# Optimization experiments

Measured on AMD Instinct MI355X. Metric: run time of the kernel, lower is better.

## Reference

```python
import jax, jax.numpy as jnp
import numpy as np

HIDDEN = 1024
INTER = 4096
N_EXPERTS = 8


def geglu(x, w1, w2, w3):
    # x: [N, C], w1/w2: [C, I], w3: [I, C]
    return (jax.nn.gelu(x @ w1, approximate=False) * (x @ w2)) @ w3


def setup_inputs() -> dict:
    key = jax.random.key(0)
    ks = jax.random.split(key, 8)
    s = 0.02
    x = jax.random.normal(ks[0], (2, 2048, HIDDEN), dtype=jnp.float32)
    w1s = jax.random.normal(ks[1], (HIDDEN, INTER), dtype=jnp.float32) * s
    w2s = jax.random.normal(ks[2], (HIDDEN, INTER), dtype=jnp.float32) * s
    w3s = jax.random.normal(ks[3], (INTER, HIDDEN), dtype=jnp.float32) * s
    W1 = jax.random.normal(ks[4], (N_EXPERTS, HIDDEN, INTER), dtype=jnp.float32) * s
    W2 = jax.random.normal(ks[5], (N_EXPERTS, HIDDEN, INTER), dtype=jnp.float32) * s
    W3 = jax.random.normal(ks[6], (N_EXPERTS, INTER, HIDDEN), dtype=jnp.float32) * s
    Wg = jax.random.normal(ks[7], (HIDDEN, N_EXPERTS), dtype=jnp.float32) * s
    return {"x": x, "w1s": w1s, "w2s": w2s, "w3s": w3s,
            "W1": W1, "W2": W2, "W3": W3, "Wg": Wg}


def reference(x, w1s, w2s, w3s, W1, W2, W3, Wg):
    B, T, C = x.shape
    xf = x.reshape(-1, C)  # [N, C]
    shared = geglu(xf, w1s, w2s, w3s)  # [N, C]
    logits = xf @ Wg  # [N, E]
    # top-1 of softmax == argmax of logits (softmax is monotone);
    # NOTE: original torch code does NOT multiply by the routing prob.
    idx = jnp.argmax(logits, axis=-1)  # [N]
    final = jnp.zeros_like(xf)
    for e in range(N_EXPERTS):  # small fixed expert count
        y = geglu(xf, W1[e], W2[e], W3[e])  # [N, C]
        final = final + jnp.where((idx == e)[:, None], y, 0.0)
    return (shared + final).reshape(B, T, C)
```

## Files before the change

### kernel.cpp

```cpp
#include <hip/hip_runtime.h>
#include <stdint.h>

#define HIDDEN 1024
#define INTER  4096
#define NTOK   4096
#define HROWS  (2*NTOK)
#define MAXB1  40
#define MAXB2  72
#define NMAT   27

typedef unsigned short u16;
typedef unsigned int   u32;
typedef __bf16  bf16x8 __attribute__((ext_vector_type(8)));
typedef float   f32x4  __attribute__((ext_vector_type(4)));
typedef u32     u32x4  __attribute__((ext_vector_type(4)));

#define WAITVM(N) asm volatile("s_waitcnt vmcnt(" #N ")" ::: "memory")

__device__ __forceinline__ void hard_barrier() {
  asm volatile("" ::: "memory");
  __builtin_amdgcn_s_barrier();
  asm volatile("" ::: "memory");
}

__device__ __forceinline__ u16 f2bf(float f) {
  u32 u = __float_as_uint(f);
  u32 r = u + 0x7FFFu + ((u >> 16) & 1u);
  return (u16)(r >> 16);
}

__device__ __forceinline__ u32 cvt_pk_bf16(float lo, float hi) {
  u32 r;
  asm("v_cvt_pk_bf16_f32 %0, %1, %2" : "=v"(r) : "v"(lo), "v"(hi));
  return r;
}

__device__ __forceinline__ void glds16(const void* g, void* l) {
  __builtin_amdgcn_global_load_lds(
      (const __attribute__((address_space(1))) void*)g,
      (__attribute__((address_space(3))) void*)l, 16, 0, 0);
}


__global__ void k_init(int* cnt, int* fill) {
  if (threadIdx.x < 8) { cnt[threadIdx.x] = 0; fill[threadIdx.x] = 0; }
}

__global__ __launch_bounds__(256) void k_gate(const float* __restrict__ x,
                                              const float* __restrict__ wg,
                                              int* __restrict__ idx,
                                              int* __restrict__ cnt) {
  int wave = threadIdx.x >> 6, lane = threadIdx.x & 63;
  int t = blockIdx.x * 4 + wave;
  if (t >= NTOK) return;
  float acc[8];
  #pragma unroll
  for (int e = 0; e < 8; ++e) acc[e] = 0.f;
  const float* xr = x + (size_t)t * HIDDEN;
  for (int c = lane; c < HIDDEN; c += 64) {
    float xv = xr[c];
    const float* wrow = wg + (size_t)c * 8;
    #pragma unroll
    for (int e = 0; e < 8; ++e) acc[e] += xv * wrow[e];
  }
  #pragma unroll
  for (int e = 0; e < 8; ++e)
    for (int s = 32; s; s >>= 1) acc[e] += __shfl_xor(acc[e], s);
  if (lane == 0) {
    int best = 0; float bv = acc[0];
    #pragma unroll
    for (int e = 1; e < 8; ++e) if (acc[e] > bv) { bv = acc[e]; best = e; }
    idx[t] = best;
    atomicAdd(&cnt[best], 1);
  }
}

__global__ void k_cvt(const float* __restrict__ x, u16* __restrict__ xb, int n4) {
  int i = blockIdx.x * blockDim.x + threadIdx.x;
  if (i >= n4) return;
  float4 v = ((const float4*)x)[i];
  ushort4 o;
  o.x = f2bf(v.x); o.y = f2bf(v.y); o.z = f2bf(v.z); o.w = f2bf(v.w);
  ((ushort4*)xb)[i] = o;
}

__global__ void k_table(const int* __restrict__ cnt, int* __restrict__ off,
                        int4* __restrict__ tab1, int* __restrict__ nblk1,
                        int4* __restrict__ tab2, int* __restrict__ nblk2) {
  if (threadIdx.x != 0 || blockIdx.x != 0) return;
  int o = 0;
  int offs[8];
  for (int e = 0; e < 8; ++e) { offs[e] = o; off[e] = o; o += cnt[e]; }
  int nb = 0;
  for (int m = 0; m < NTOK / 256; ++m)
    tab1[nb++] = make_int4(8, m * 256, 256, 0);
  for (int e = 0; e < 8; ++e)
    for (int j = 0; j * 256 < cnt[e]; ++j) {
      int rows = cnt[e] - j * 256; if (rows > 256) rows = 256;
      tab1[nb++] = make_int4(e, NTOK + offs[e] + j * 256, rows, offs[e] + j * 256);
    }
  *nblk1 = nb;
  nb = 0;
  for (int m = 0; m < NTOK / 128; ++m)
    tab2[nb++] = make_int4(8, m * 128, 128, 0);
  for (int e = 0; e < 8; ++e)
    for (int j = 0; j * 128 < cnt[e]; ++j) {
      int rows = cnt[e] - j * 128; if (rows > 128) rows = 128;
      tab2[nb++] = make_int4(e, NTOK + offs[e] + j * 128, rows, offs[e] + j * 128);
    }
  *nblk2 = nb;
}

__global__ void k_scatter(const int* __restrict__ idx, const int* __restrict__ off,
                          int* __restrict__ fill, int* __restrict__ perm) {
  int t = blockIdx.x * blockDim.x + threadIdx.x;
  if (t >= NTOK) return;
  int e = idx[t];
  int p = atomicAdd(&fill[e], 1);
  perm[off[e] + p] = t;
}


__global__ __launch_bounds__(256) void k_wcvt(
    const float* __restrict__ w1s, const float* __restrict__ w2s,
    const float* __restrict__ w3s, const float* __restrict__ W1,
    const float* __restrict__ W2,  const float* __restrict__ W3,
    u16* __restrict__ Wb)
{
  int bid = blockIdx.x;
  int m = bid >> 9, pair = bid & 511;
  const float* src; int N, nkt, kt, pp2;
  if (m < 18) {
    N = INTER; nkt = 32;
    int mm = (m < 9) ? m : m - 9;
    const float* sp = (m < 9) ? w1s : w2s;
    const float* ep = (m < 9) ? W1 : W2;
    src = (mm == 0) ? sp : ep + (size_t)(mm - 1) * HIDDEN * INTER;
    kt = pair >> 4; pp2 = pair & 15;
  } else {
    N = HIDDEN; nkt = 128;
    int mm = m - 18;
    src = (mm == 0) ? w3s : W3 + (size_t)(mm - 1) * INTER * HIDDEN;
    kt = pair >> 2; pp2 = pair & 3;
  }

  __shared__ float tileF[32 * 256];
  int tid = threadIdx.x;
  const float* in0 = src + (size_t)(kt * 32) * N + pp2 * 256;
  #pragma unroll
  for (int i = 0; i < 8; ++i) {
    int f = tid + 256 * i;
    int k = f >> 6, c4 = f & 63;
    *(float4*)&tileF[k * 256 + c4 * 4] = *(const float4*)(in0 + (size_t)k * N + c4 * 4);
  }
  __syncthreads();

  int p2 = tid >> 7, n = tid & 127;
  int pidx = m * 1024 + (pp2 * 2 + p2) * nkt + kt;
  u16* outp = Wb + (size_t)pidx * 4096 + n * 32;
  #pragma unroll
  for (int s = 0; s < 4; ++s) {
    int k8 = s ^ ((n >> 1) & 3);
    const float* col = &tileF[(k8 * 8) * 256 + p2 * 128 + n];
    u32x4 pk;
    pk.x = cvt_pk_bf16(col[0],    col[256]);
    pk.y = cvt_pk_bf16(col[512],  col[768]);
    pk.z = cvt_pk_bf16(col[1024], col[1280]);
    pk.w = cvt_pk_bf16(col[1536], col[1792]);
    *(u32x4*)(outp + s * 8) = pk;
  }
}


#define MLP1_TILE(B, STG, WN)                                                        \
  do {                                                                               \
    const u16* LA = pAr  + (B) * 16384;                                              \
    const u16* L1 = pBr1 + (B) * 16384;                                              \
    const u16* L2 = pBr2 + (B) * 16384;                                              \
    bf16x8 af[8], f1[2], f2[2];                                                      \
    _Pragma("unroll")                                                                \
    for (int mi = 0; mi < 4; ++mi) af[mi] = *(const bf16x8*)(LA + mi * 512);         \
    _Pragma("unroll")                                                                \
    for (int ni = 0; ni < 2; ++ni) {                                                 \
      f1[ni] = *(const bf16x8*)(L1 + ni * 512);                                      \
      f2[ni] = *(const bf16x8*)(L2 + ni * 512);                                      \
    }                                                                                \
    if (STG) {                                                                       \
      char* Ld = smem + (((B) + 3) & 3) * 32768;                                     \
      glds16(srcA0, Ld + w * 2048);                                                  \
      glds16(srcA1, Ld + w * 2048 + 1024);                                           \
      srcA0 += 64; srcA1 += 64;                                                      \
    }                                                                                \
    __builtin_amdgcn_s_setprio(1);                                                   \
    _Pragma("unroll")                                                                \
    for (int mi = 0; mi < 4; ++mi) {                                                 \
      acc1[mi][0] = __builtin_amdgcn_mfma_f32_16x16x32_bf16(af[mi], f1[0], acc1[mi][0], 0, 0, 0); \
      acc1[mi][1] = __builtin_amdgcn_mfma_f32_16x16x32_bf16(af[mi], f1[1], acc1[mi][1], 0, 0, 0); \
      acc2[mi][0] = __builtin_amdgcn_mfma_f32_16x16x32_bf16(af[mi], f2[0], acc2[mi][0], 0, 0, 0); \
      acc2[mi][1] = __builtin_amdgcn_mfma_f32_16x16x32_bf16(af[mi], f2[1], acc2[mi][1], 0, 0, 0); \
    }                                                                                \
    __builtin_amdgcn_s_setprio(0);                                                   \
    hard_barrier();                                                                  \
    _Pragma("unroll")                                                                \
    for (int mi = 4; mi < 8; ++mi) af[mi] = *(const bf16x8*)(LA + mi * 512);         \
    if (STG) {                                                                       \
      char* Ld = smem + (((B) + 3) & 3) * 32768;                                     \
      glds16(srcB1, Ld + 16384 + w * 1024);                                          \
      glds16(srcB2, Ld + 24576 + w * 1024);                                          \
      srcB1 += 8192; srcB2 += 8192;                                                  \
    }                                                                                \
    __builtin_amdgcn_s_setprio(1);                                                   \
    _Pragma("unroll")                                                                \
    for (int mi = 4; mi < 8; ++mi) {                                                 \
      acc1[mi][0] = __builtin_amdgcn_mfma_f32_16x16x32_bf16(af[mi], f1[0], acc1[mi][0], 0, 0, 0); \
      acc1[mi][1] = __builtin_amdgcn_mfma_f32_16x16x32_bf16(af[mi], f1[1], acc1[mi][1], 0, 0, 0); \
      acc2[mi][0] = __builtin_amdgcn_mfma_f32_16x16x32_bf16(af[mi], f2[0], acc2[mi][0], 0, 0, 0); \
      acc2[mi][1] = __builtin_amdgcn_mfma_f32_16x16x32_bf16(af[mi], f2[1], acc2[mi][1], 0, 0, 0); \
    }                                                                                \
    __builtin_amdgcn_s_setprio(0);                                                   \
    WN;                                                                              \
    hard_barrier();                                                                  \
  } while (0)

__global__ __launch_bounds__(512, 2) void k_mlp1(
    const u16* __restrict__ xb, const u16* __restrict__ Wb,
    const int* __restrict__ perm, const int4* __restrict__ tab,
    const int* __restrict__ nblk, u16* __restrict__ Hbuf)
{
  int bx = blockIdx.x;
  if (bx >= *nblk) return;
  int4 te = tab[bx];
  int g = te.x, hrow0 = te.y, rows = te.z, pb = te.w;
  int m1 = (g == 8) ? 0 : 1 + g;
  int pp = blockIdx.y;
  int nbase = pp * 128;

  extern __shared__ __align__(16) char smem[];
  int tid = threadIdx.x;
  int w = tid >> 6, lane = tid & 63;
  int q = lane >> 4, rl = lane & 15;
  int mw = w >> 2, nw = w & 3;

  int tokj[2];
  #pragma unroll
  for (int j = 0; j < 2; ++j) {
    int r = w * 32 + j * 16 + (lane >> 2);
    int rc = (r < rows) ? r : (rows - 1);
    tokj[j] = (g == 8) ? (hrow0 + rc) : perm[pb + rc];
  }
  int gch = ((lane & 3) ^ ((lane >> 3) & 3)) * 16;

  const char* srcA0 = (const char*)xb + (size_t)tokj[0] * 2048 + gch;
  const char* srcA1 = (const char*)xb + (size_t)tokj[1] * 2048 + gch;
  const char* srcB1 = (const char*)Wb + ((size_t)m1 * 1024 + pp * 32) * 8192 + (tid << 4);
  const char* srcB2 = (const char*)Wb + ((size_t)(m1 + 9) * 1024 + pp * 32) * 8192 + (tid << 4);

  int co = (q ^ ((rl >> 1) & 3)) * 8;
  const u16* pAr  = (const u16*)smem + (mw * 128 + rl) * 32 + co;
  const u16* pBr1 = (const u16*)smem + 8192  + (nw * 32 + rl) * 32 + co;
  const u16* pBr2 = (const u16*)smem + 12288 + (nw * 32 + rl) * 32 + co;

  f32x4 acc1[8][2], acc2[8][2];
  f32x4 z = {0.f, 0.f, 0.f, 0.f};
  #pragma unroll
  for (int mi = 0; mi < 8; ++mi)
    #pragma unroll
    for (int ni = 0; ni < 2; ++ni) { acc1[mi][ni] = z; acc2[mi][ni] = z; }

  #pragma unroll
  for (int p = 0; p < 3; ++p) {
    char* Ld = smem + p * 32768;
    glds16(srcA0, Ld + w * 2048);
    glds16(srcA1, Ld + w * 2048 + 1024);
    srcA0 += 64; srcA1 += 64;
    glds16(srcB1, Ld + 16384 + w * 1024);
    glds16(srcB2, Ld + 24576 + w * 1024);
    srcB1 += 8192; srcB2 += 8192;
  }
  WAITVM(8);
  hard_barrier();

  for (int t0 = 0; t0 < 28; t0 += 4) {
    MLP1_TILE(0, 1, WAITVM(8));
    MLP1_TILE(1, 1, WAITVM(8));
    MLP1_TILE(2, 1, WAITVM(8));
    MLP1_TILE(3, 1, WAITVM(8));
  }
  MLP1_TILE(0, 1, WAITVM(8));
  MLP1_TILE(1, 0, WAITVM(4));
  MLP1_TILE(2, 0, WAITVM(0));
  MLP1_TILE(3, 0, (void)0);

  #pragma unroll
  for (int mi = 0; mi < 8; ++mi) {
    #pragma unroll
    for (int j = 0; j < 4; ++j) {
      int r = mw * 128 + mi * 16 + q * 4 + j;
      if (r < rows) {
        size_t hb = (size_t)(hrow0 + r) * INTER + nbase + nw * 32;
        #pragma unroll
        for (int ni = 0; ni < 2; ++ni) {
          float h1 = acc1[mi][ni][j];
          float h2 = acc2[mi][ni][j];
          float ge = 0.5f * h1 * (1.0f + erff(h1 * 0.7071067811865476f));
          Hbuf[hb + ni * 16 + rl] = f2bf(ge * h2);
        }
      }
    }
  }
}


#define MLP2_TILE(B, STG, WN)                                                        \
  do {                                                                               \
    const u16* LA = pAr + (B) * 12288;                                               \
    const u16* LB = pBr + (B) * 12288;                                               \
    bf16x8 af[4], bf[4];                                                             \
    _Pragma("unroll")                                                                \
    for (int mi = 0; mi < 4; ++mi) af[mi] = *(const bf16x8*)(LA + mi * 512);         \
    _Pragma("unroll")                                                                \
    for (int ni = 0; ni < 4; ++ni) bf[ni] = *(const bf16x8*)(LB + ni * 512);         \
    if (STG) {                                                                       \
      char* Ld = smem + (((B) + 3) & 3) * 24576;                                     \
      glds16(srcA0, Ld + w * 1024);              srcA0 += 64;                        \
      glds16(srcB0, Ld + 8192 + w * 1024);       srcB0 += 8192;                      \
      glds16(srcB1, Ld + 16384 + w * 1024);      srcB1 += 8192;                      \
    }                                                                                \
    __builtin_amdgcn_s_setprio(1);                                                   \
    _Pragma("unroll")                                                                \
    for (int mi = 0; mi < 4; ++mi)                                                   \
      _Pragma("unroll")                                                              \
      for (int ni = 0; ni < 4; ++ni)                                                 \
        acc[mi][ni] = __builtin_amdgcn_mfma_f32_16x16x32_bf16(af[mi], bf[ni], acc[mi][ni], 0, 0, 0); \
    __builtin_amdgcn_s_setprio(0);                                                   \
    WN;                                                                              \
    hard_barrier();                                                                  \
  } while (0)

__global__ __launch_bounds__(512, 2) void k_mlp2(
    const u16* __restrict__ Hbuf, const u16* __restrict__ Wb,
    const int* __restrict__ perm, const int4* __restrict__ tab,
    const int* __restrict__ nblk, float* __restrict__ out,
    float* __restrict__ yexp)
{
  int bx = blockIdx.x;
  if (bx >= *nblk) return;
  int4 te = tab[bx];
  int g = te.x, hrow0 = te.y, rows = te.z, pb = te.w;
  int m3 = (g == 8) ? 18 : 19 + g;
  int pp2 = blockIdx.y;

  extern __shared__ __align__(16) char smem[];
  int tid = threadIdx.x;
  int w = tid >> 6, lane = tid & 63;
  int q = lane >> 4, rl = lane & 15;
  int mw = w >> 2, nw = w & 3;

  int rr = w * 16 + (lane >> 2);
  int rc = (rr < rows) ? rr : (rows - 1);
  int hr = hrow0 + rc;
  int gch = ((lane & 3) ^ ((lane >> 3) & 3)) * 16;

  const char* srcA0 = (const char*)Hbuf + (size_t)hr * (INTER * 2) + gch;
  const char* srcB0 = (const char*)Wb + ((size_t)m3 * 1024 + (pp2 * 2) * 128) * 8192 + (tid << 4);
  const char* srcB1 = (const char*)Wb + ((size_t)m3 * 1024 + (pp2 * 2 + 1) * 128) * 8192 + (tid << 4);

  int co = (q ^ ((rl >> 1) & 3)) * 8;
  const u16* pAr = (const u16*)smem + (mw * 64 + rl) * 32 + co;
  const u16* pBr = (const u16*)smem + 4096 + (nw * 64 + rl) * 32 + co;

  f32x4 acc[4][4];
  f32x4 z = {0.f, 0.f, 0.f, 0.f};
  #pragma unroll
  for (int mi = 0; mi < 4; ++mi)
    #pragma unroll
    for (int ni = 0; ni < 4; ++ni) acc[mi][ni] = z;

  #pragma unroll
  for (int p = 0; p < 3; ++p) {
    char* Ld = smem + p * 24576;
    glds16(srcA0, Ld + w * 1024);          srcA0 += 64;
    glds16(srcB0, Ld + 8192 + w * 1024);   srcB0 += 8192;
    glds16(srcB1, Ld + 16384 + w * 1024);  srcB1 += 8192;
  }
  WAITVM(6);
  hard_barrier();

  for (int t0 = 0; t0 < 124; t0 += 4) {
    MLP2_TILE(0, 1, WAITVM(6));
    MLP2_TILE(1, 1, WAITVM(6));
    MLP2_TILE(2, 1, WAITVM(6));
    MLP2_TILE(3, 1, WAITVM(6));
  }
  MLP2_TILE(0, 1, WAITVM(6));
  MLP2_TILE(1, 0, WAITVM(3));
  MLP2_TILE(2, 0, WAITVM(0));
  MLP2_TILE(3, 0, (void)0);

  float* dstb = (g == 8) ? out : yexp;
  #pragma unroll
  for (int mi = 0; mi < 4; ++mi) {
    #pragma unroll
    for (int j = 0; j < 4; ++j) {
      int r = mw * 64 + mi * 16 + q * 4 + j;
      if (r < rows) {
        int tok = (g == 8) ? (hrow0 + r) : perm[pb + r];
        size_t ob = (size_t)tok * HIDDEN + pp2 * 256 + nw * 64;
        #pragma unroll
        for (int ni = 0; ni < 4; ++ni)
          dstb[ob + ni * 16 + rl] = acc[mi][ni][j];
      }
    }
  }
}

__global__ void k_add(float* __restrict__ out, const float* __restrict__ yexp, int n4) {
  int i = blockIdx.x * blockDim.x + threadIdx.x;
  if (i >= n4) return;
  float4 a = ((const float4*)out)[i];
  float4 b = ((const float4*)yexp)[i];
  a.x += b.x; a.y += b.y; a.z += b.z; a.w += b.w;
  ((float4*)out)[i] = a;
}


extern "C" void kernel_launch(void* const* d_in, const int* in_sizes, int n_in,
                              void* d_out, int out_size, void* d_ws, size_t ws_size,
                              hipStream_t stream) {
  const float* x   = (const float*)d_in[0];
  const float* w1s = (const float*)d_in[1];
  const float* w2s = (const float*)d_in[2];
  const float* w3s = (const float*)d_in[3];
  const float* W1  = (const float*)d_in[4];
  const float* W2  = (const float*)d_in[5];
  const float* W3  = (const float*)d_in[6];
  const float* Wg  = (const float*)d_in[7];
  float* out = (float*)d_out;

  char* ws = (char*)d_ws;
  size_t o_xb   = 0;
  size_t o_H    = o_xb   + (size_t)NTOK * HIDDEN * 2;
  size_t o_yexp = o_H    + (size_t)HROWS * INTER * 2;
  size_t o_Wb   = o_yexp + (size_t)NTOK * HIDDEN * 4;
  size_t o_idx  = o_Wb   + (size_t)NMAT * 1024 * 8192;
  size_t o_perm = o_idx  + (size_t)NTOK * 4;
  size_t o_cnt  = o_perm + (size_t)NTOK * 4;
  size_t o_off  = o_cnt  + 32;
  size_t o_fill = o_off  + 32;
  size_t o_nb1  = o_fill + 32;
  size_t o_nb2  = o_nb1  + 32;
  size_t o_tab1 = o_nb2  + 32;
  size_t o_tab2 = o_tab1 + (size_t)MAXB1 * 16;
  size_t need   = o_tab2 + (size_t)MAXB2 * 16;
  if (ws_size < need) return;

  u16*  xb   = (u16*)(ws + o_xb);
  u16*  Hbuf = (u16*)(ws + o_H);
  float* yexp = (float*)(ws + o_yexp);
  u16*  Wb   = (u16*)(ws + o_Wb);
  int*  idx  = (int*)(ws + o_idx);
  int*  perm = (int*)(ws + o_perm);
  int*  cnt  = (int*)(ws + o_cnt);
  int*  off  = (int*)(ws + o_off);
  int*  fill = (int*)(ws + o_fill);
  int*  nblk1 = (int*)(ws + o_nb1);
  int*  nblk2 = (int*)(ws + o_nb2);
  int4* tab1 = (int4*)(ws + o_tab1);
  int4* tab2 = (int4*)(ws + o_tab2);

  k_init<<<1, 64, 0, stream>>>(cnt, fill);
  k_gate<<<NTOK / 4, 256, 0, stream>>>(x, Wg, idx, cnt);
  k_cvt<<<(NTOK * HIDDEN / 4) / 256, 256, 0, stream>>>(x, xb, NTOK * HIDDEN / 4);
  k_wcvt<<<NMAT * 512, 256, 0, stream>>>(w1s, w2s, w3s, W1, W2, W3, Wb);
  k_table<<<1, 1, 0, stream>>>(cnt, off, tab1, nblk1, tab2, nblk2);
  k_scatter<<<NTOK / 256, 256, 0, stream>>>(idx, off, fill, perm);
  k_mlp1<<<dim3(MAXB1, INTER / 128), 512, 131072, stream>>>(xb, Wb, perm, tab1, nblk1, Hbuf);
  k_mlp2<<<dim3(MAXB2, HIDDEN / 256), 512, 98304, stream>>>(Hbuf, Wb, perm, tab2, nblk2, out, yexp);
  k_add<<<(NTOK * HIDDEN / 4) / 256, 256, 0, stream>>>(out, yexp, NTOK * HIDDEN / 4);
}
```

Baseline: 524.0 us.

## Prefetch next-stage LDS fragments into registers and tighten vmcnt waits in MLP kernels

Both GEMM kernels now load the next k-stage's LDS operand fragments into registers during the current stage's MFMAs. k_mlp1 staggers the A/B fragment reads across the barrier halves, and k_mlp2 ping-pongs two register fragment sets. The vmcnt waits are tightened so the next staged buffer is ready before it is read ahead. This aims to hide LDS read latency behind MFMA execution, at the cost of higher register pressure that could hurt occupancy at launch_bounds(512,2).

```diff
diff --git a/kernel.cpp b/kernel.cpp
--- a/kernel.cpp
+++ b/kernel.cpp
@@ -172,19 +172,17 @@
 }
 
 
-#define MLP1_TILE(B, STG, WN)                                                        \
+#define M1_TILE(B, STG, RD, WN)                                                      \
   do {                                                                               \
-    const u16* LA = pAr  + (B) * 16384;                                              \
-    const u16* L1 = pBr1 + (B) * 16384;                                              \
-    const u16* L2 = pBr2 + (B) * 16384;                                              \
-    bf16x8 af[8], f1[2], f2[2];                                                      \
-    _Pragma("unroll")                                                                \
-    for (int mi = 0; mi < 4; ++mi) af[mi] = *(const bf16x8*)(LA + mi * 512);         \
-    _Pragma("unroll")                                                                \
-    for (int ni = 0; ni < 2; ++ni) {                                                 \
-      f1[ni] = *(const bf16x8*)(L1 + ni * 512);                                      \
-      f2[ni] = *(const bf16x8*)(L2 + ni * 512);                                      \
-    }                                                                                \
+    const u16* LA  = pAr  + (B) * 16384;                                             \
+    const u16* LAn = pAr  + (((B) + 1) & 3) * 16384;                                 \
+    const u16* L1n = pBr1 + (((B) + 1) & 3) * 16384;                                 \
+    const u16* L2n = pBr2 + (((B) + 1) & 3) * 16384;                                 \
+                            \
+    af[4] = *(const bf16x8*)(LA + 4 * 512);                                          \
+    af[5] = *(const bf16x8*)(LA + 5 * 512);                                          \
+    af[6] = *(const bf16x8*)(LA + 6 * 512);                                          \
+    af[7] = *(const bf16x8*)(LA + 7 * 512);                                          \
     if (STG) {                                                                       \
       char* Ld = smem + (((B) + 3) & 3) * 32768;                                     \
       glds16(srcA0, Ld + w * 2048);                                                  \
@@ -201,8 +199,13 @@
     }                                                                                \
     __builtin_amdgcn_s_setprio(0);                                                   \
     hard_barrier();                                                                  \
-    _Pragma("unroll")                                                                \
-    for (int mi = 4; mi < 8; ++mi) af[mi] = *(const bf16x8*)(LA + mi * 512);         \
+          \
+    if (RD) {                                                                        \
+      af[0] = *(const bf16x8*)(LAn);                                                 \
+      af[1] = *(const bf16x8*)(LAn + 512);                                           \
+      af[2] = *(const bf16x8*)(LAn + 2 * 512);                                       \
+      af[3] = *(const bf16x8*)(LAn + 3 * 512);                                       \
+    }                                                                                \
     if (STG) {                                                                       \
       char* Ld = smem + (((B) + 3) & 3) * 32768;                                     \
       glds16(srcB1, Ld + 16384 + w * 1024);                                          \
@@ -218,6 +221,13 @@
       acc2[mi][1] = __builtin_amdgcn_mfma_f32_16x16x32_bf16(af[mi], f2[1], acc2[mi][1], 0, 0, 0); \
     }                                                                                \
     __builtin_amdgcn_s_setprio(0);                                                   \
+    \
+    if (RD) {                                                                        \
+      f1[0] = *(const bf16x8*)(L1n);                                                 \
+      f1[1] = *(const bf16x8*)(L1n + 512);                                           \
+      f2[0] = *(const bf16x8*)(L2n);                                                 \
+      f2[1] = *(const bf16x8*)(L2n + 512);                                           \
+    }                                                                                \
     WN;                                                                              \
     hard_barrier();                                                                  \
   } while (0)
@@ -277,19 +287,29 @@
     glds16(srcB2, Ld + 24576 + w * 1024);
     srcB1 += 8192; srcB2 += 8192;
   }
-  WAITVM(8);
+  WAITVM(4);
   hard_barrier();
 
-  for (int t0 = 0; t0 < 28; t0 += 4) {
-    MLP1_TILE(0, 1, WAITVM(8));
-    MLP1_TILE(1, 1, WAITVM(8));
-    MLP1_TILE(2, 1, WAITVM(8));
-    MLP1_TILE(3, 1, WAITVM(8));
-  }
-  MLP1_TILE(0, 1, WAITVM(8));
-  MLP1_TILE(1, 0, WAITVM(4));
-  MLP1_TILE(2, 0, WAITVM(0));
-  MLP1_TILE(3, 0, (void)0);
+  bf16x8 af[8], f1[2], f2[2];
+  af[0] = *(const bf16x8*)(pAr);
+  af[1] = *(const bf16x8*)(pAr + 512);
+  af[2] = *(const bf16x8*)(pAr + 2 * 512);
+  af[3] = *(const bf16x8*)(pAr + 3 * 512);
+  f1[0] = *(const bf16x8*)(pBr1);
+  f1[1] = *(const bf16x8*)(pBr1 + 512);
+  f2[0] = *(const bf16x8*)(pBr2);
+  f2[1] = *(const bf16x8*)(pBr2 + 512);
+
+  for (int t0 = 0; t0 < 7; ++t0) {
+    M1_TILE(0, 1, 1, WAITVM(4));
+    M1_TILE(1, 1, 1, WAITVM(4));
+    M1_TILE(2, 1, 1, WAITVM(4));
+    M1_TILE(3, 1, 1, WAITVM(4));
+  }
+  M1_TILE(0, 1, 1, WAITVM(4));
+  M1_TILE(1, 0, 1, WAITVM(0));
+  M1_TILE(2, 0, 1, (void)0);
+  M1_TILE(3, 0, 0, (void)0);
 
   #pragma unroll
   for (int mi = 0; mi < 8; ++mi) {
@@ -311,15 +331,20 @@
 }
 
 
-#define MLP2_TILE(B, STG, WN)                                                        \
+#define M2_TILE(B, CUR, NXT, STG, RD, WN)                                            \
   do {                                                                               \
-    const u16* LA = pAr + (B) * 12288;                                               \
-    const u16* LB = pBr + (B) * 12288;                                               \
-    bf16x8 af[4], bf[4];                                                             \
-    _Pragma("unroll")                                                                \
-    for (int mi = 0; mi < 4; ++mi) af[mi] = *(const bf16x8*)(LA + mi * 512);         \
-    _Pragma("unroll")                                                                \
-    for (int ni = 0; ni < 4; ++ni) bf[ni] = *(const bf16x8*)(LB + ni * 512);         \
+    const u16* LAn = pAr + (((B) + 1) & 3) * 12288;                                  \
+    const u16* LBn = pBr + (((B) + 1) & 3) * 12288;                                  \
+    if (RD) {                                                                        \
+      af##NXT[0] = *(const bf16x8*)(LAn);                                            \
+      af##NXT[1] = *(const bf16x8*)(LAn + 512);                                      \
+      af##NXT[2] = *(const bf16x8*)(LAn + 2 * 512);                                  \
+      af##NXT[3] = *(const bf16x8*)(LAn + 3 * 512);                                  \
+      bf##NXT[0] = *(const bf16x8*)(LBn);                                            \
+      bf##NXT[1] = *(const bf16x8*)(LBn + 512);                                      \
+      bf##NXT[2] = *(const bf16x8*)(LBn + 2 * 512);                                  \
+      bf##NXT[3] = *(const bf16x8*)(LBn + 3 * 512);                                  \
+    }                                                                                \
     if (STG) {                                                                       \
       char* Ld = smem + (((B) + 3) & 3) * 24576;                                     \
       glds16(srcA0, Ld + w * 1024);              srcA0 += 64;                        \
@@ -331,7 +356,7 @@
     for (int mi = 0; mi < 4; ++mi)                                                   \
       _Pragma("unroll")                                                              \
       for (int ni = 0; ni < 4; ++ni)                                                 \
-        acc[mi][ni] = __builtin_amdgcn_mfma_f32_16x16x32_bf16(af[mi], bf[ni], acc[mi][ni], 0, 0, 0); \
+        acc[mi][ni] = __builtin_amdgcn_mfma_f32_16x16x32_bf16(af##CUR[mi], bf##CUR[ni], acc[mi][ni], 0, 0, 0); \
     __builtin_amdgcn_s_setprio(0);                                                   \
     WN;                                                                              \
     hard_barrier();                                                                  \
@@ -383,19 +408,29 @@
     glds16(srcB0, Ld + 8192 + w * 1024);   srcB0 += 8192;
     glds16(srcB1, Ld + 16384 + w * 1024);  srcB1 += 8192;
   }
-  WAITVM(6);
+  WAITVM(3);
   hard_barrier();
 
-  for (int t0 = 0; t0 < 124; t0 += 4) {
-    MLP2_TILE(0, 1, WAITVM(6));
-    MLP2_TILE(1, 1, WAITVM(6));
-    MLP2_TILE(2, 1, WAITVM(6));
-    MLP2_TILE(3, 1, WAITVM(6));
-  }
-  MLP2_TILE(0, 1, WAITVM(6));
-  MLP2_TILE(1, 0, WAITVM(3));
-  MLP2_TILE(2, 0, WAITVM(0));
-  MLP2_TILE(3, 0, (void)0);
+  bf16x8 afA[4], bfA[4], afB[4], bfB[4];
+  afA[0] = *(const bf16x8*)(pAr);
+  afA[1] = *(const bf16x8*)(pAr + 512);
+  afA[2] = *(const bf16x8*)(pAr + 2 * 512);
+  afA[3] = *(const bf16x8*)(pAr + 3 * 512);
+  bfA[0] = *(const bf16x8*)(pBr);
+  bfA[1] = *(const bf16x8*)(pBr + 512);
+  bfA[2] = *(const bf16x8*)(pBr + 2 * 512);
+  bfA[3] = *(const bf16x8*)(pBr + 3 * 512);
+
+  for (int t0 = 0; t0 < 31; ++t0) {
+    M2_TILE(0, A, B, 1, 1, WAITVM(3));
+    M2_TILE(1, B, A, 1, 1, WAITVM(3));
+    M2_TILE(2, A, B, 1, 1, WAITVM(3));
+    M2_TILE(3, B, A, 1, 1, WAITVM(3));
+  }
+  M2_TILE(0, A, B, 1, 1, WAITVM(3));
+  M2_TILE(1, B, A, 0, 1, WAITVM(0));
+  M2_TILE(2, A, B, 0, 1, (void)0);
+  M2_TILE(3, B, A, 0, 0, (void)0);
 
   float* dstb = (g == 8) ? out : yexp;
   #pragma unroll
```

After: 532.6 us. About the same (+1.6%).

## Shrink MLP GEMM tiles to 128 rows with 4-wave blocks and triple buffering

Applied to the files above, without the earlier changes.

Both expert GEMM kernels move from 512-thread blocks with 256-row (mlp1) or 256-column (mlp2) tiles to 256-thread blocks with 128x128 tiles, sharing one 128-row routing table. The LDS pipeline drops from 4 stages to 3, and all loads are issued at the start of each tile rather than split around a mid-tile barrier. Smaller tiles mean less padding waste on partial expert blocks, more blocks to fill the CUs, and lower LDS use per block so more blocks fit per CU. The cost is less operand reuse per loaded byte and a shallower prefetch pipeline.

```diff
diff --git a/kernel.cpp b/kernel.cpp
--- a/kernel.cpp
+++ b/kernel.cpp
@@ -5,8 +5,7 @@
 #define INTER  4096
 #define NTOK   4096
 #define HROWS  (2*NTOK)
-#define MAXB1  40
-#define MAXB2  72
+#define MAXB   72
 #define NMAT   27
 
 typedef unsigned short u16;
@@ -85,30 +84,20 @@
 }
 
 __global__ void k_table(const int* __restrict__ cnt, int* __restrict__ off,
-                        int4* __restrict__ tab1, int* __restrict__ nblk1,
-                        int4* __restrict__ tab2, int* __restrict__ nblk2) {
+                        int4* __restrict__ tab, int* __restrict__ nblk) {
   if (threadIdx.x != 0 || blockIdx.x != 0) return;
   int o = 0;
   int offs[8];
   for (int e = 0; e < 8; ++e) { offs[e] = o; off[e] = o; o += cnt[e]; }
   int nb = 0;
-  for (int m = 0; m < NTOK / 256; ++m)
-    tab1[nb++] = make_int4(8, m * 256, 256, 0);
-  for (int e = 0; e < 8; ++e)
-    for (int j = 0; j * 256 < cnt[e]; ++j) {
-      int rows = cnt[e] - j * 256; if (rows > 256) rows = 256;
-      tab1[nb++] = make_int4(e, NTOK + offs[e] + j * 256, rows, offs[e] + j * 256);
-    }
-  *nblk1 = nb;
-  nb = 0;
   for (int m = 0; m < NTOK / 128; ++m)
-    tab2[nb++] = make_int4(8, m * 128, 128, 0);
+    tab[nb++] = make_int4(8, m * 128, 128, 0);
   for (int e = 0; e < 8; ++e)
     for (int j = 0; j * 128 < cnt[e]; ++j) {
       int rows = cnt[e] - j * 128; if (rows > 128) rows = 128;
-      tab2[nb++] = make_int4(e, NTOK + offs[e] + j * 128, rows, offs[e] + j * 128);
+      tab[nb++] = make_int4(e, NTOK + offs[e] + j * 128, rows, offs[e] + j * 128);
     }
-  *nblk2 = nb;
+  *nblk = nb;
 }
 
 __global__ void k_scatter(const int* __restrict__ idx, const int* __restrict__ off,
@@ -172,57 +161,43 @@
 }
 
 
-#define MLP1_TILE(B, STG, WN)                                                        \
+#define M1_TILE(B, STG, WN)                                                          \
   do {                                                                               \
-    const u16* LA = pAr  + (B) * 16384;                                              \
-    const u16* L1 = pBr1 + (B) * 16384;                                              \
-    const u16* L2 = pBr2 + (B) * 16384;                                              \
-    bf16x8 af[8], f1[2], f2[2];                                                      \
-    _Pragma("unroll")                                                                \
-    for (int mi = 0; mi < 4; ++mi) af[mi] = *(const bf16x8*)(LA + mi * 512);         \
-    _Pragma("unroll")                                                                \
-    for (int ni = 0; ni < 2; ++ni) {                                                 \
-      f1[ni] = *(const bf16x8*)(L1 + ni * 512);                                      \
-      f2[ni] = *(const bf16x8*)(L2 + ni * 512);                                      \
-    }                                                                                \
+    const u16* LA = pAr  + (B) * 12288;                                              \
+    const u16* L1 = pBr1 + (B) * 12288;                                              \
+    const u16* L2 = pBr2 + (B) * 12288;                                              \
     if (STG) {                                                                       \
-      char* Ld = smem + (((B) + 3) & 3) * 32768;                                     \
+      char* Ld = smem + (((B) + 2) % 3) * 24576;                                     \
       glds16(srcA0, Ld + w * 2048);                                                  \
       glds16(srcA1, Ld + w * 2048 + 1024);                                           \
-      srcA0 += 64; srcA1 += 64;                                                      \
+      glds16(srcB1, Ld + 8192 + w * 2048);                                           \
+      glds16(srcB1 + 1024, Ld + 8192 + w * 2048 + 1024);                             \
+      glds16(srcB2, Ld + 16384 + w * 2048);                                          \
+      glds16(srcB2 + 1024, Ld + 16384 + w * 2048 + 1024);                            \
+      srcA0 += 64; srcA1 += 64; srcB1 += 8192; srcB2 += 8192;                        \
+    }                                                                                \
+    bf16x8 af[4], b1[4], b2[4];                                                      \
+    _Pragma("unroll")                                                                \
+    for (int mi = 0; mi < 4; ++mi) af[mi] = *(const bf16x8*)(LA + mi * 512);         \
+    _Pragma("unroll")                                                                \
+    for (int ni = 0; ni < 4; ++ni) {                                                 \
+      b1[ni] = *(const bf16x8*)(L1 + ni * 512);                                      \
+      b2[ni] = *(const bf16x8*)(L2 + ni * 512);                                      \
     }                                                                                \
     __builtin_amdgcn_s_setprio(1);                                                   \
     _Pragma("unroll")                                                                \
-    for (int mi = 0; mi < 4; ++mi) {                                                 \
-      acc1[mi][0] = __builtin_amdgcn_mfma_f32_16x16x32_bf16(af[mi], f1[0], acc1[mi][0], 0, 0, 0); \
-      acc1[mi][1] = __builtin_amdgcn_mfma_f32_16x16x32_bf16(af[mi], f1[1], acc1[mi][1], 0, 0, 0); \
-      acc2[mi][0] = __builtin_amdgcn_mfma_f32_16x16x32_bf16(af[mi], f2[0], acc2[mi][0], 0, 0, 0); \
-      acc2[mi][1] = __builtin_amdgcn_mfma_f32_16x16x32_bf16(af[mi], f2[1], acc2[mi][1], 0, 0, 0); \
-    }                                                                                \
-    __builtin_amdgcn_s_setprio(0);                                                   \
-    hard_barrier();                                                                  \
-    _Pragma("unroll")                                                                \
-    for (int mi = 4; mi < 8; ++mi) af[mi] = *(const bf16x8*)(LA + mi * 512);         \
-    if (STG) {                                                                       \
-      char* Ld = smem + (((B) + 3) & 3) * 32768;                                     \
-      glds16(srcB1, Ld + 16384 + w * 1024);                                          \
-      glds16(srcB2, Ld + 24576 + w * 1024);                                          \
-      srcB1 += 8192; srcB2 += 8192;                                                  \
-    }                                                                                \
-    __builtin_amdgcn_s_setprio(1);                                                   \
-    _Pragma("unroll")                                                                \
-    for (int mi = 4; mi < 8; ++mi) {                                                 \
-      acc1[mi][0] = __builtin_amdgcn_mfma_f32_16x16x32_bf16(af[mi], f1[0], acc1[mi][0], 0, 0, 0); \
-      acc1[mi][1] = __builtin_amdgcn_mfma_f32_16x16x32_bf16(af[mi], f1[1], acc1[mi][1], 0, 0, 0); \
-      acc2[mi][0] = __builtin_amdgcn_mfma_f32_16x16x32_bf16(af[mi], f2[0], acc2[mi][0], 0, 0, 0); \
-      acc2[mi][1] = __builtin_amdgcn_mfma_f32_16x16x32_bf16(af[mi], f2[1], acc2[mi][1], 0, 0, 0); \
-    }                                                                                \
+    for (int mi = 0; mi < 4; ++mi)                                                   \
+      _Pragma("unroll")                                                              \
+      for (int ni = 0; ni < 4; ++ni) {                                               \
+        acc1[mi][ni] = __builtin_amdgcn_mfma_f32_16x16x32_bf16(af[mi], b1[ni], acc1[mi][ni], 0, 0, 0); \
+        acc2[mi][ni] = __builtin_amdgcn_mfma_f32_16x16x32_bf16(af[mi], b2[ni], acc2[mi][ni], 0, 0, 0); \
+      }                                                                              \
     __builtin_amdgcn_s_setprio(0);                                                   \
     WN;                                                                              \
     hard_barrier();                                                                  \
   } while (0)
 
-__global__ __launch_bounds__(512, 2) void k_mlp1(
+__global__ __launch_bounds__(256, 2) void k_mlp1(
     const u16* __restrict__ xb, const u16* __restrict__ Wb,
     const int* __restrict__ perm, const int4* __restrict__ tab,
     const int* __restrict__ nblk, u16* __restrict__ Hbuf)
@@ -239,7 +214,7 @@
   int tid = threadIdx.x;
   int w = tid >> 6, lane = tid & 63;
   int q = lane >> 4, rl = lane & 15;
-  int mw = w >> 2, nw = w & 3;
+  int mw = w >> 1, nw = w & 1;
 
   int tokj[2];
   #pragma unroll
@@ -252,54 +227,52 @@
 
   const char* srcA0 = (const char*)xb + (size_t)tokj[0] * 2048 + gch;
   const char* srcA1 = (const char*)xb + (size_t)tokj[1] * 2048 + gch;
-  const char* srcB1 = (const char*)Wb + ((size_t)m1 * 1024 + pp * 32) * 8192 + (tid << 4);
-  const char* srcB2 = (const char*)Wb + ((size_t)(m1 + 9) * 1024 + pp * 32) * 8192 + (tid << 4);
+  const char* srcB1 = (const char*)Wb + ((size_t)m1 * 1024 + pp * 32) * 8192 + w * 2048 + (lane << 4);
+  const char* srcB2 = (const char*)Wb + ((size_t)(m1 + 9) * 1024 + pp * 32) * 8192 + w * 2048 + (lane << 4);
 
   int co = (q ^ ((rl >> 1) & 3)) * 8;
-  const u16* pAr  = (const u16*)smem + (mw * 128 + rl) * 32 + co;
-  const u16* pBr1 = (const u16*)smem + 8192  + (nw * 32 + rl) * 32 + co;
-  const u16* pBr2 = (const u16*)smem + 12288 + (nw * 32 + rl) * 32 + co;
-
-  f32x4 acc1[8][2], acc2[8][2];
+  const u16* pAr  = (const u16*)smem + (mw * 64 + rl) * 32 + co;
+  const u16* pBr1 = (const u16*)smem + 4096 + (nw * 64 + rl) * 32 + co;
+  const u16* pBr2 = (const u16*)smem + 8192 + (nw * 64 + rl) * 32 + co;
+
+  f32x4 acc1[4][4], acc2[4][4];
   f32x4 z = {0.f, 0.f, 0.f, 0.f};
   #pragma unroll
-  for (int mi = 0; mi < 8; ++mi)
-    #pragma unroll
-    for (int ni = 0; ni < 2; ++ni) { acc1[mi][ni] = z; acc2[mi][ni] = z; }
-
-  #pragma unroll
-  for (int p = 0; p < 3; ++p) {
-    char* Ld = smem + p * 32768;
+  for (int mi = 0; mi < 4; ++mi)
+    #pragma unroll
+    for (int ni = 0; ni < 4; ++ni) { acc1[mi][ni] = z; acc2[mi][ni] = z; }
+
+  #pragma unroll
+  for (int p = 0; p < 2; ++p) {
+    char* Ld = smem + p * 24576;
     glds16(srcA0, Ld + w * 2048);
     glds16(srcA1, Ld + w * 2048 + 1024);
-    srcA0 += 64; srcA1 += 64;
-    glds16(srcB1, Ld + 16384 + w * 1024);
-    glds16(srcB2, Ld + 24576 + w * 1024);
-    srcB1 += 8192; srcB2 += 8192;
-  }
-  WAITVM(8);
+    glds16(srcB1, Ld + 8192 + w * 2048);
+    glds16(srcB1 + 1024, Ld + 8192 + w * 2048 + 1024);
+    glds16(srcB2, Ld + 16384 + w * 2048);
+    glds16(srcB2 + 1024, Ld + 16384 + w * 2048 + 1024);
+    srcA0 += 64; srcA1 += 64; srcB1 += 8192; srcB2 += 8192;
+  }
+  WAITVM(6);
   hard_barrier();
 
-  for (int t0 = 0; t0 < 28; t0 += 4) {
-    MLP1_TILE(0, 1, WAITVM(8));
-    MLP1_TILE(1, 1, WAITVM(8));
-    MLP1_TILE(2, 1, WAITVM(8));
-    MLP1_TILE(3, 1, WAITVM(8));
-  }
-  MLP1_TILE(0, 1, WAITVM(8));
-  MLP1_TILE(1, 0, WAITVM(4));
-  MLP1_TILE(2, 0, WAITVM(0));
-  MLP1_TILE(3, 0, (void)0);
-
-  #pragma unroll
-  for (int mi = 0; mi < 8; ++mi) {
+  for (int r = 0; r < 10; ++r) {
+    M1_TILE(0, 1, WAITVM(6));
+    M1_TILE(1, 1, WAITVM(6));
+    M1_TILE(2, 1, WAITVM(6));
+  }
+  M1_TILE(0, 0, WAITVM(0));
+  M1_TILE(1, 0, (void)0);
+
+  #pragma unroll
+  for (int mi = 0; mi < 4; ++mi) {
     #pragma unroll
     for (int j = 0; j < 4; ++j) {
-      int r = mw * 128 + mi * 16 + q * 4 + j;
+      int r = mw * 64 + mi * 16 + q * 4 + j;
       if (r < rows) {
-        size_t hb = (size_t)(hrow0 + r) * INTER + nbase + nw * 32;
+        size_t hb = (size_t)(hrow0 + r) * INTER + nbase + nw * 64;
         #pragma unroll
-        for (int ni = 0; ni < 2; ++ni) {
+        for (int ni = 0; ni < 4; ++ni) {
           float h1 = acc1[mi][ni][j];
           float h2 = acc2[mi][ni][j];
           float ge = 0.5f * h1 * (1.0f + erff(h1 * 0.7071067811865476f));
@@ -311,21 +284,23 @@
 }
 
 
-#define MLP2_TILE(B, STG, WN)                                                        \
+#define M2_TILE(B, STG, WN)                                                          \
   do {                                                                               \
-    const u16* LA = pAr + (B) * 12288;                                               \
-    const u16* LB = pBr + (B) * 12288;                                               \
+    const u16* LA = pAr + (B) * 8192;                                                \
+    const u16* LB = pBr + (B) * 8192;                                                \
+    if (STG) {                                                                       \
+      char* Ld = smem + (((B) + 2) % 3) * 16384;                                     \
+      glds16(srcA0, Ld + w * 2048);                                                  \
+      glds16(srcA1, Ld + w * 2048 + 1024);                                           \
+      glds16(srcB0, Ld + 8192 + w * 2048);                                           \
+      glds16(srcB0 + 1024, Ld + 8192 + w * 2048 + 1024);                             \
+      srcA0 += 64; srcA1 += 64; srcB0 += 8192;                                       \
+    }                                                                                \
     bf16x8 af[4], bf[4];                                                             \
     _Pragma("unroll")                                                                \
     for (int mi = 0; mi < 4; ++mi) af[mi] = *(const bf16x8*)(LA + mi * 512);         \
     _Pragma("unroll")                                                                \
     for (int ni = 0; ni < 4; ++ni) bf[ni] = *(const bf16x8*)(LB + ni * 512);         \
-    if (STG) {                                                                       \
-      char* Ld = smem + (((B) + 3) & 3) * 24576;                                     \
-      glds16(srcA0, Ld + w * 1024);              srcA0 += 64;                        \
-      glds16(srcB0, Ld + 8192 + w * 1024);       srcB0 += 8192;                      \
-      glds16(srcB1, Ld + 16384 + w * 1024);      srcB1 += 8192;                      \
-    }                                                                                \
     __builtin_amdgcn_s_setprio(1);                                                   \
     _Pragma("unroll")                                                                \
     for (int mi = 0; mi < 4; ++mi)                                                   \
@@ -337,7 +312,7 @@
     hard_barrier();                                                                  \
   } while (0)
 
-__global__ __launch_bounds__(512, 2) void k_mlp2(
+__global__ __launch_bounds__(256, 3) void k_mlp2(
     const u16* __restrict__ Hbuf, const u16* __restrict__ Wb,
     const int* __restrict__ perm, const int4* __restrict__ tab,
     const int* __restrict__ nblk, float* __restrict__ out,
@@ -348,22 +323,27 @@
   int4 te = tab[bx];
   int g = te.x, hrow0 = te.y, rows = te.z, pb = te.w;
   int m3 = (g == 8) ? 18 : 19 + g;
-  int pp2 = blockIdx.y;
+  int pp = blockIdx.y;
+  int nbase = pp * 128;
 
   extern __shared__ __align__(16) char smem[];
   int tid = threadIdx.x;
   int w = tid >> 6, lane = tid & 63;
   int q = lane >> 4, rl = lane & 15;
-  int mw = w >> 2, nw = w & 3;
-
-  int rr = w * 16 + (lane >> 2);
-  int rc = (rr < rows) ? rr : (rows - 1);
-  int hr = hrow0 + rc;
+  int mw = w >> 1, nw = w & 1;
+
+  int hr[2];
+  #pragma unroll
+  for (int j = 0; j < 2; ++j) {
+    int r = w * 32 + j * 16 + (lane >> 2);
+    int rc = (r < rows) ? r : (rows - 1);
+    hr[j] = hrow0 + rc;
+  }
   int gch = ((lane & 3) ^ ((lane >> 3) & 3)) * 16;
 
-  const char* srcA0 = (const char*)Hbuf + (size_t)hr * (INTER * 2) + gch;
-  const char* srcB0 = (const char*)Wb + ((size_t)m3 * 1024 + (pp2 * 2) * 128) * 8192 + (tid << 4);
-  const char* srcB1 = (const char*)Wb + ((size_t)m3 * 1024 + (pp2 * 2 + 1) * 128) * 8192 + (tid << 4);
+  const char* srcA0 = (const char*)Hbuf + (size_t)hr[0] * (INTER * 2) + gch;
+  const char* srcA1 = (const char*)Hbuf + (size_t)hr[1] * (INTER * 2) + gch;
+  const char* srcB0 = (const char*)Wb + ((size_t)m3 * 1024 + pp * 128) * 8192 + w * 2048 + (lane << 4);
 
   int co = (q ^ ((rl >> 1) & 3)) * 8;
   const u16* pAr = (const u16*)smem + (mw * 64 + rl) * 32 + co;
@@ -377,25 +357,24 @@
     for (int ni = 0; ni < 4; ++ni) acc[mi][ni] = z;
 
   #pragma unroll
-  for (int p = 0; p < 3; ++p) {
-    char* Ld = smem + p * 24576;
-    glds16(srcA0, Ld + w * 1024);          srcA0 += 64;
-    glds16(srcB0, Ld + 8192 + w * 1024);   srcB0 += 8192;
-    glds16(srcB1, Ld + 16384 + w * 1024);  srcB1 += 8192;
-  }
-  WAITVM(6);
+  for (int p = 0; p < 2; ++p) {
+    char* Ld = smem + p * 16384;
+    glds16(srcA0, Ld + w * 2048);
+    glds16(srcA1, Ld + w * 2048 + 1024);
+    glds16(srcB0, Ld + 8192 + w * 2048);
+    glds16(srcB0 + 1024, Ld + 8192 + w * 2048 + 1024);
+    srcA0 += 64; srcA1 += 64; srcB0 += 8192;
+  }
+  WAITVM(4);
   hard_barrier();
 
-  for (int t0 = 0; t0 < 124; t0 += 4) {
-    MLP2_TILE(0, 1, WAITVM(6));
-    MLP2_TILE(1, 1, WAITVM(6));
-    MLP2_TILE(2, 1, WAITVM(6));
-    MLP2_TILE(3, 1, WAITVM(6));
-  }
-  MLP2_TILE(0, 1, WAITVM(6));
-  MLP2_TILE(1, 0, WAITVM(3));
-  MLP2_TILE(2, 0, WAITVM(0));
-  MLP2_TILE(3, 0, (void)0);
+  for (int r = 0; r < 42; ++r) {
+    M2_TILE(0, 1, WAITVM(4));
+    M2_TILE(1, 1, WAITVM(4));
+    M2_TILE(2, 1, WAITVM(4));
+  }
+  M2_TILE(0, 0, WAITVM(0));
+  M2_TILE(1, 0, (void)0);
 
   float* dstb = (g == 8) ? out : yexp;
   #pragma unroll
@@ -405,7 +384,7 @@
       int r = mw * 64 + mi * 16 + q * 4 + j;
       if (r < rows) {
         int tok = (g == 8) ? (hrow0 + r) : perm[pb + r];
-        size_t ob = (size_t)tok * HIDDEN + pp2 * 256 + nw * 64;
+        size_t ob = (size_t)tok * HIDDEN + nbase + nw * 64;
         #pragma unroll
         for (int ni = 0; ni < 4; ++ni)
           dstb[ob + ni * 16 + rl] = acc[mi][ni][j];
@@ -447,11 +426,9 @@
   size_t o_cnt  = o_perm + (size_t)NTOK * 4;
   size_t o_off  = o_cnt  + 32;
   size_t o_fill = o_off  + 32;
-  size_t o_nb1  = o_fill + 32;
-  size_t o_nb2  = o_nb1  + 32;
-  size_t o_tab1 = o_nb2  + 32;
-  size_t o_tab2 = o_tab1 + (size_t)MAXB1 * 16;
-  size_t need   = o_tab2 + (size_t)MAXB2 * 16;
+  size_t o_nblk = o_fill + 32;
+  size_t o_tab  = o_nblk + 32;
+  size_t need   = o_tab  + (size_t)MAXB * 16;
   if (ws_size < need) return;
 
   u16*  xb   = (u16*)(ws + o_xb);
@@ -463,18 +440,16 @@
   int*  cnt  = (int*)(ws + o_cnt);
   int*  off  = (int*)(ws + o_off);
   int*  fill = (int*)(ws + o_fill);
-  int*  nblk1 = (int*)(ws + o_nb1);
-  int*  nblk2 = (int*)(ws + o_nb2);
-  int4* tab1 = (int4*)(ws + o_tab1);
-  int4* tab2 = (int4*)(ws + o_tab2);
+  int*  nblk = (int*)(ws + o_nblk);
+  int4* tab  = (int4*)(ws + o_tab);
 
   k_init<<<1, 64, 0, stream>>>(cnt, fill);
   k_gate<<<NTOK / 4, 256, 0, stream>>>(x, Wg, idx, cnt);
   k_cvt<<<(NTOK * HIDDEN / 4) / 256, 256, 0, stream>>>(x, xb, NTOK * HIDDEN / 4);
   k_wcvt<<<NMAT * 512, 256, 0, stream>>>(w1s, w2s, w3s, W1, W2, W3, Wb);
-  k_table<<<1, 1, 0, stream>>>(cnt, off, tab1, nblk1, tab2, nblk2);
+  k_table<<<1, 1, 0, stream>>>(cnt, off, tab, nblk);
   k_scatter<<<NTOK / 256, 256, 0, stream>>>(idx, off, fill, perm);
-  k_mlp1<<<dim3(MAXB1, INTER / 128), 512, 131072, stream>>>(xb, Wb, perm, tab1, nblk1, Hbuf);
-  k_mlp2<<<dim3(MAXB2, HIDDEN / 256), 512, 98304, stream>>>(Hbuf, Wb, perm, tab2, nblk2, out, yexp);
+  k_mlp1<<<dim3(MAXB, INTER / 128), 256, 73728, stream>>>(xb, Wb, perm, tab, nblk, Hbuf);
+  k_mlp2<<<dim3(MAXB, HIDDEN / 128), 256, 49152, stream>>>(Hbuf, Wb, perm, tab, nblk, out, yexp);
   k_add<<<(NTOK * HIDDEN / 4) / 256, 256, 0, stream>>>(out, yexp, NTOK * HIDDEN / 4);
 }
```

Result: no change. 532.1 us (+1.5%).
